# Performance work log

Measured on AMD Instinct MI355X. Metric: run time of the kernel, lower is better.

## Reference

```python
import jax, jax.numpy as jnp
import numpy as np

B, V, FIN, COUT, K = 16, 20000, 64, 64, 16


def setup_inputs() -> dict:
    key = jax.random.key(0)
    k1, k2, k3, k4 = jax.random.split(key, 4)
    x = jax.random.normal(k1, (B, V, FIN), dtype=jnp.float32)
    Wx = jax.random.normal(k2, (FIN, COUT), dtype=jnp.float32) * (1.0 / np.sqrt(FIN))
    Wn = jax.random.normal(k3, (FIN, COUT), dtype=jnp.float32) * (1.0 / np.sqrt(FIN))
    b = jnp.zeros((COUT,), dtype=jnp.float32)
    # neighbor indices into the padded input: 0 is the zero-padding row, 1..V are real vertices
    neighbor = jax.random.randint(k4, (V, K), 0, V + 1, dtype=jnp.int32)
    return {"x": x, "Wx": Wx, "Wn": Wn, "b": b, "neighbor": neighbor}


def reference(x, Wx, Wn, b, neighbor):
    # x: [B, V, Fin]; neighbor: [V, K] indices into padded (V+1) vertex axis
    Bsz, Vn, Fin = x.shape
    pad = jnp.zeros((Bsz, 1, Fin), dtype=x.dtype)
    padded = jnp.concatenate([pad, x], axis=1)            # [B, V+1, Fin]
    nb = padded[:, neighbor, :]                            # [B, V, K, Fin] (gather)
    nb_mean = jnp.mean(nb, axis=2)                         # sum/K == mean (zeros included)
    out = jnp.einsum('bvf,fc->bvc', x, Wx) \
        + jnp.einsum('bvf,fc->bvc', nb_mean, Wn) + b
    return out
```

## Files before the change

kernel.cpp:

```cpp
#include <hip/hip_runtime.h>
#include <hip/hip_bf16.h>

#define BATCH 16
#define NV    20000
#define FIN   64
#define NCOUT 64
#define NK    16
#define TOTROWS  (BATCH * NV)
#define NTILES   (TOTROWS / 16)
#define TPX      (NTILES / 8)

typedef __attribute__((ext_vector_type(8))) short bf16x8;
typedef __attribute__((ext_vector_type(4))) float f32x4;
typedef __attribute__((ext_vector_type(4))) unsigned short u16x4;

__device__ __forceinline__ short f2b(float f) {
    __hip_bfloat16 h = __float2bfloat16(f);
    return __builtin_bit_cast(short, h);
}

__global__ __launch_bounds__(256, 4) void convnet_gemm(
    const float* __restrict__ x,
    const float* __restrict__ Wx,
    const float* __restrict__ Wn,
    const float* __restrict__ bias,
    __hip_bfloat16* __restrict__ z,
    float* __restrict__ out)
{
    const int lane = threadIdx.x & 63;
    const int m    = lane & 15;
    const int quad = lane >> 4;

    bf16x8 bf[8][2];
#pragma unroll
    for (int t = 0; t < 8; ++t) {
        const float* W = (t < 4) ? Wx : Wn;
        const float scale = (t < 4) ? 1.0f : (1.0f / 16.0f);
        const int c = 4 * m + (t & 3);
#pragma unroll
        for (int h = 0; h < 2; ++h) {
            bf16x8 fr;
#pragma unroll
            for (int j = 0; j < 8; ++j) {
                const int f = 32 * h + quad * 8 + j;
                fr[j] = f2b(W[f * NCOUT + c] * scale);
            }
            bf[t][h] = fr;
        }
    }
    float bias_q[4];
#pragma unroll
    for (int t = 0; t < 4; ++t) bias_q[t] = bias[4 * m + t];

    const int xcd = blockIdx.x & 7;
    const int bi  = blockIdx.x >> 3;
    const int wl  = bi * 4 + ((int)threadIdx.x >> 6);
    const int WPX = (gridDim.x >> 3) * 4;

    for (int t0 = wl; t0 < TPX; t0 += WPX) {
        const int rt = __builtin_amdgcn_readfirstlane(xcd * TPX + t0);
        const float* xt =
            x + (size_t)rt * (16 * FIN) + (size_t)m * FIN + quad * 8;

        const float4 La0 = ((const float4*)xt)[0];
        const float4 La1 = ((const float4*)xt)[1];
        const float4 Lb0 = ((const float4*)(xt + 32))[0];
        const float4 Lb1 = ((const float4*)(xt + 32))[1];

        bf16x8 af0, af1;
        af0[0] = f2b(La0.x); af0[1] = f2b(La0.y); af0[2] = f2b(La0.z); af0[3] = f2b(La0.w);
        af0[4] = f2b(La1.x); af0[5] = f2b(La1.y); af0[6] = f2b(La1.z); af0[7] = f2b(La1.w);
        af1[0] = f2b(Lb0.x); af1[1] = f2b(Lb0.y); af1[2] = f2b(Lb0.z); af1[3] = f2b(Lb0.w);
        af1[4] = f2b(Lb1.x); af1[5] = f2b(Lb1.y); af1[6] = f2b(Lb1.z); af1[7] = f2b(Lb1.w);

        const size_t rbase = (size_t)rt * 16 + quad * 4;

        {
            f32x4 accP[4];
#pragma unroll
            for (int t = 0; t < 4; ++t) accP[t] = (f32x4){0.f, 0.f, 0.f, 0.f};
#pragma unroll
            for (int t = 0; t < 4; ++t)
                accP[t] = __builtin_amdgcn_mfma_f32_16x16x32_bf16(af0, bf[t][0], accP[t], 0, 0, 0);
#pragma unroll
            for (int t = 0; t < 4; ++t)
                accP[t] = __builtin_amdgcn_mfma_f32_16x16x32_bf16(af1, bf[t][1], accP[t], 0, 0, 0);
#pragma unroll
            for (int r = 0; r < 4; ++r) {
                const size_t orow = (rbase + r) * NCOUT + 4 * m;
                float4 o;
                o.x = accP[0][r] + bias_q[0];
                o.y = accP[1][r] + bias_q[1];
                o.z = accP[2][r] + bias_q[2];
                o.w = accP[3][r] + bias_q[3];
                *(float4*)(out + orow) = o;
            }
        }
        {
            f32x4 accZ[4];
#pragma unroll
            for (int t = 0; t < 4; ++t) accZ[t] = (f32x4){0.f, 0.f, 0.f, 0.f};
#pragma unroll
            for (int t = 0; t < 4; ++t)
                accZ[t] = __builtin_amdgcn_mfma_f32_16x16x32_bf16(af0, bf[t + 4][0], accZ[t], 0, 0, 0);
#pragma unroll
            for (int t = 0; t < 4; ++t)
                accZ[t] = __builtin_amdgcn_mfma_f32_16x16x32_bf16(af1, bf[t + 4][1], accZ[t], 0, 0, 0);
#pragma unroll
            for (int r = 0; r < 4; ++r) {
                const size_t orow = (rbase + r) * NCOUT + 4 * m;
                u16x4 zz;
                zz.x = (unsigned short)f2b(accZ[0][r]);
                zz.y = (unsigned short)f2b(accZ[1][r]);
                zz.z = (unsigned short)f2b(accZ[2][r]);
                zz.w = (unsigned short)f2b(accZ[3][r]);
                *(u16x4*)(z + orow) = zz;
            }
        }
    }
}

__global__ __launch_bounds__(256, 8) void convnet_gather(
    const int* __restrict__ nbr,
    const __hip_bfloat16* __restrict__ z,
    float* __restrict__ out)
{
    const int lane = threadIdx.x & 63;
    const int s    = lane >> 4;
    const int c    = lane & 15;
    const int xcd  = blockIdx.x & 7;
    const int bi   = blockIdx.x >> 3;
    const int wl   = bi * 4 + ((int)threadIdx.x >> 6);
    const int WPX  = (gridDim.x >> 3) * 4;

    const int zcol   = c * 8;
    const int GROUPS = (2 * NV) / 4;

    for (int g = wl; g < GROUPS; g += WPX) {
        const int gu = __builtin_amdgcn_readfirstlane(g);
        const int bl = (gu >= NV / 4) ? 1 : 0;
        const int b  = 2 * xcd + bl;
        const int v0 = gu * 4 - bl * NV;
        const int row0 = b * NV + v0;

        float4* o = (float4*)(out + (size_t)(row0 + s) * NCOUT + 4 * c);
        float4 ov = *o;

        const int4* nb4 =
            (const int4*)((const char*)nbr + (size_t)(v0 + s) * (NK * 4));
        const int4 i0 = nb4[0];
        const int4 i1 = nb4[1];
        const int4 i2 = nb4[2];
        const int4 i3 = nb4[3];
        int id[NK];
        id[0] = i0.x; id[1] = i0.y; id[2]  = i0.z; id[3]  = i0.w;
        id[4] = i1.x; id[5] = i1.y; id[6]  = i1.z; id[7]  = i1.w;
        id[8] = i2.x; id[9] = i2.y; id[10] = i2.z; id[11] = i2.w;
        id[12] = i3.x; id[13] = i3.y; id[14] = i3.z; id[15] = i3.w;

        const char* zb = (const char*)z + (size_t)b * NV * 128;
        float a0 = 0.f, a1 = 0.f, a2 = 0.f, a3 = 0.f;
#pragma unroll
        for (int k = 0; k < NK; ++k) {
            const int idx = id[k];
            int sel = idx - 1;
            sel = sel < 0 ? 0 : sel;
            const uint2 d = *(const uint2*)(zb + (size_t)(unsigned)(sel * 128 + zcol));
            const unsigned dx = idx ? d.x : 0u;
            const unsigned dy = idx ? d.y : 0u;
            a0 += __builtin_bit_cast(float, dx << 16);
            a1 += __builtin_bit_cast(float, dx & 0xFFFF0000u);
            a2 += __builtin_bit_cast(float, dy << 16);
            a3 += __builtin_bit_cast(float, dy & 0xFFFF0000u);
        }

        ov.x += a0; ov.y += a1; ov.z += a2; ov.w += a3;
        *o = ov;
    }
}

extern "C" void kernel_launch(void* const* d_in, const int* in_sizes, int n_in,
                              void* d_out, int out_size, void* d_ws, size_t ws_size,
                              hipStream_t stream) {
    const float* x    = (const float*)d_in[0];
    const float* Wx   = (const float*)d_in[1];
    const float* Wn   = (const float*)d_in[2];
    const float* bias = (const float*)d_in[3];
    const int*   nbr  = (const int*)d_in[4];
    float* out = (float*)d_out;

    __hip_bfloat16* z = (__hip_bfloat16*)d_ws;

    hipLaunchKernelGGL(convnet_gemm, dim3(1024), dim3(256), 0, stream,
                       x, Wx, Wn, bias, z, out);
    hipLaunchKernelGGL(convnet_gather, dim3(2048), dim3(256), 0, stream,
                       nbr, z, out);
}
```

Baseline: 232.1 us.

## Fuse gather into Wx GEMM pass, split z precompute into separate kernel

Splits work into a z-only pass (x·Wn/16 stored as bf16) and a fused kernel that recomputes x·Wx, gathers neighbor z rows, adds bias and writes out once. This removes the intermediate write and re-read of the fp32 output between kernels, at the cost of reading x twice. Loads and stores of streaming data use nontemporal hints, and the fused kernel walks tiles in reverse order, perhaps to hit cache on recently read x. Mixing the gather with MFMA work in one kernel may cut occupancy or latency hiding.

Result: slower. 269.9 us (+16.3%).

```diff
diff --git a/kernel.cpp b/kernel.cpp
--- a/kernel.cpp
+++ b/kernel.cpp
@@ -9,43 +9,113 @@
 #define TOTROWS  (BATCH * NV)
 #define NTILES   (TOTROWS / 16)
 #define TPX      (NTILES / 8)
+#define TPB      (NV / 16)
 
 typedef __attribute__((ext_vector_type(8))) short bf16x8;
 typedef __attribute__((ext_vector_type(4))) float f32x4;
 typedef __attribute__((ext_vector_type(4))) unsigned short u16x4;
+typedef __attribute__((ext_vector_type(2))) unsigned int u32x2;
 
 __device__ __forceinline__ short f2b(float f) {
     __hip_bfloat16 h = __float2bfloat16(f);
     return __builtin_bit_cast(short, h);
 }
 
-__global__ __launch_bounds__(256, 4) void convnet_gemm(
+__global__ __launch_bounds__(256, 4) void convnet_zpass(
+    const float* __restrict__ x,
+    const float* __restrict__ Wn,
+    __hip_bfloat16* __restrict__ z)
+{
+    const int lane = threadIdx.x & 63;
+    const int m    = lane & 15;
+    const int quad = lane >> 4;
+
+    bf16x8 bn[4][2];
+#pragma unroll
+    for (int t = 0; t < 4; ++t) {
+        const int c = 4 * m + t;
+#pragma unroll
+        for (int h = 0; h < 2; ++h) {
+            bf16x8 fr;
+#pragma unroll
+            for (int j = 0; j < 8; ++j) {
+                const int f = 32 * h + quad * 8 + j;
+                fr[j] = f2b(Wn[f * NCOUT + c] * (1.0f / 16.0f));
+            }
+            bn[t][h] = fr;
+        }
+    }
+
+    const int xcd = blockIdx.x & 7;
+    const int bi  = blockIdx.x >> 3;
+    const int wl  = bi * 4 + ((int)threadIdx.x >> 6);
+    const int WPX = (gridDim.x >> 3) * 4;
+
+    for (int t0 = wl; t0 < TPX; t0 += WPX) {
+        const int rt = __builtin_amdgcn_readfirstlane(xcd * TPX + t0);
+        const float* xt =
+            x + (size_t)rt * (16 * FIN) + (size_t)m * FIN + quad * 8;
+
+        const f32x4 La0 = __builtin_nontemporal_load((const f32x4*)xt);
+        const f32x4 La1 = __builtin_nontemporal_load((const f32x4*)xt + 1);
+        const f32x4 Lb0 = __builtin_nontemporal_load((const f32x4*)(xt + 32));
+        const f32x4 Lb1 = __builtin_nontemporal_load((const f32x4*)(xt + 32) + 1);
+
+        bf16x8 af0, af1;
+        af0[0] = f2b(La0.x); af0[1] = f2b(La0.y); af0[2] = f2b(La0.z); af0[3] = f2b(La0.w);
+        af0[4] = f2b(La1.x); af0[5] = f2b(La1.y); af0[6] = f2b(La1.z); af0[7] = f2b(La1.w);
+        af1[0] = f2b(Lb0.x); af1[1] = f2b(Lb0.y); af1[2] = f2b(Lb0.z); af1[3] = f2b(Lb0.w);
+        af1[4] = f2b(Lb1.x); af1[5] = f2b(Lb1.y); af1[6] = f2b(Lb1.z); af1[7] = f2b(Lb1.w);
+
+        f32x4 acc[4];
+#pragma unroll
+        for (int t = 0; t < 4; ++t) acc[t] = (f32x4){0.f, 0.f, 0.f, 0.f};
+#pragma unroll
+        for (int t = 0; t < 4; ++t)
+            acc[t] = __builtin_amdgcn_mfma_f32_16x16x32_bf16(af0, bn[t][0], acc[t], 0, 0, 0);
+#pragma unroll
+        for (int t = 0; t < 4; ++t)
+            acc[t] = __builtin_amdgcn_mfma_f32_16x16x32_bf16(af1, bn[t][1], acc[t], 0, 0, 0);
+
+        const size_t rbase = (size_t)rt * 16 + quad * 4;
+#pragma unroll
+        for (int r = 0; r < 4; ++r) {
+            const size_t orow = (rbase + r) * NCOUT + 4 * m;
+            u16x4 zz;
+            zz.x = (unsigned short)f2b(acc[0][r]);
+            zz.y = (unsigned short)f2b(acc[1][r]);
+            zz.z = (unsigned short)f2b(acc[2][r]);
+            zz.w = (unsigned short)f2b(acc[3][r]);
+            *(u16x4*)(z + orow) = zz;
+        }
+    }
+}
+
+__global__ __launch_bounds__(256, 4) void convnet_fused(
     const float* __restrict__ x,
     const float* __restrict__ Wx,
-    const float* __restrict__ Wn,
     const float* __restrict__ bias,
-    __hip_bfloat16* __restrict__ z,
+    const int* __restrict__ nbr,
+    const __hip_bfloat16* __restrict__ z,
     float* __restrict__ out)
 {
     const int lane = threadIdx.x & 63;
     const int m    = lane & 15;
     const int quad = lane >> 4;
 
-    bf16x8 bf[8][2];
-#pragma unroll
-    for (int t = 0; t < 8; ++t) {
-        const float* W = (t < 4) ? Wx : Wn;
-        const float scale = (t < 4) ? 1.0f : (1.0f / 16.0f);
-        const int c = 4 * m + (t & 3);
+    bf16x8 bx[4][2];
+#pragma unroll
+    for (int t = 0; t < 4; ++t) {
+        const int c = 4 * m + t;
 #pragma unroll
         for (int h = 0; h < 2; ++h) {
             bf16x8 fr;
 #pragma unroll
             for (int j = 0; j < 8; ++j) {
                 const int f = 32 * h + quad * 8 + j;
-                fr[j] = f2b(W[f * NCOUT + c] * scale);
+                fr[j] = f2b(Wx[f * NCOUT + c]);
             }
-            bf[t][h] = fr;
+            bx[t][h] = fr;
         }
     }
     float bias_q[4];
@@ -57,15 +127,19 @@
     const int wl  = bi * 4 + ((int)threadIdx.x >> 6);
     const int WPX = (gridDim.x >> 3) * 4;
 
-    for (int t0 = wl; t0 < TPX; t0 += WPX) {
-        const int rt = __builtin_amdgcn_readfirstlane(xcd * TPX + t0);
+    for (int t0 = TPX - 1 - wl; t0 >= 0; t0 -= WPX) {
+        const int t0u = __builtin_amdgcn_readfirstlane(t0);
+        const int rt  = xcd * TPX + t0u;
+        const int blh = (t0u >= TPB) ? 1 : 0;
+        const int b   = 2 * xcd + blh;
+        const int v0  = (t0u - blh * TPB) * 16;
+
         const float* xt =
             x + (size_t)rt * (16 * FIN) + (size_t)m * FIN + quad * 8;
-
-        const float4 La0 = ((const float4*)xt)[0];
-        const float4 La1 = ((const float4*)xt)[1];
-        const float4 Lb0 = ((const float4*)(xt + 32))[0];
-        const float4 Lb1 = ((const float4*)(xt + 32))[1];
+        const f32x4 La0 = __builtin_nontemporal_load((const f32x4*)xt);
+        const f32x4 La1 = __builtin_nontemporal_load((const f32x4*)xt + 1);
+        const f32x4 Lb0 = __builtin_nontemporal_load((const f32x4*)(xt + 32));
+        const f32x4 Lb1 = __builtin_nontemporal_load((const f32x4*)(xt + 32) + 1);
 
         bf16x8 af0, af1;
         af0[0] = f2b(La0.x); af0[1] = f2b(La0.y); af0[2] = f2b(La0.z); af0[3] = f2b(La0.w);
@@ -73,109 +147,64 @@
         af1[0] = f2b(Lb0.x); af1[1] = f2b(Lb0.y); af1[2] = f2b(Lb0.z); af1[3] = f2b(Lb0.w);
         af1[4] = f2b(Lb1.x); af1[5] = f2b(Lb1.y); af1[6] = f2b(Lb1.z); af1[7] = f2b(Lb1.w);
 
+        f32x4 acc[4];
+#pragma unroll
+        for (int t = 0; t < 4; ++t) acc[t] = (f32x4){0.f, 0.f, 0.f, 0.f};
+#pragma unroll
+        for (int t = 0; t < 4; ++t)
+            acc[t] = __builtin_amdgcn_mfma_f32_16x16x32_bf16(af0, bx[t][0], acc[t], 0, 0, 0);
+#pragma unroll
+        for (int t = 0; t < 4; ++t)
+            acc[t] = __builtin_amdgcn_mfma_f32_16x16x32_bf16(af1, bx[t][1], acc[t], 0, 0, 0);
+
+        const char* zb = (const char*)z + (size_t)b * (NV * 128);
+        const int zcol = m * 8;
+#pragma unroll
+        for (int r = 0; r < 4; ++r) {
+            const int v = v0 + quad * 4 + r;
+            const int4* nb4 = (const int4*)nbr + (size_t)v * 4;
+            const int4 i0 = nb4[0];
+            const int4 i1 = nb4[1];
+            const int4 i2 = nb4[2];
+            const int4 i3 = nb4[3];
+            int id[NK];
+            id[0]  = i0.x; id[1]  = i0.y; id[2]  = i0.z; id[3]  = i0.w;
+            id[4]  = i1.x; id[5]  = i1.y; id[6]  = i1.z; id[7]  = i1.w;
+            id[8]  = i2.x; id[9]  = i2.y; id[10] = i2.z; id[11] = i2.w;
+            id[12] = i3.x; id[13] = i3.y; id[14] = i3.z; id[15] = i3.w;
+
+            float a0 = 0.f, a1 = 0.f, a2 = 0.f, a3 = 0.f;
+#pragma unroll
+            for (int k = 0; k < NK; ++k) {
+                const int idx = id[k];
+                int sel = idx - 1;
+                sel = sel < 0 ? 0 : sel;
+                const u32x2 d =
+                    *(const u32x2*)(zb + (size_t)(unsigned)(sel * 128 + zcol));
+                const unsigned dx = idx ? d.x : 0u;
+                const unsigned dy = idx ? d.y : 0u;
+                a0 += __builtin_bit_cast(float, dx << 16);
+                a1 += __builtin_bit_cast(float, dx & 0xFFFF0000u);
+                a2 += __builtin_bit_cast(float, dy << 16);
+                a3 += __builtin_bit_cast(float, dy & 0xFFFF0000u);
+            }
+            acc[0][r] += a0;
+            acc[1][r] += a1;
+            acc[2][r] += a2;
+            acc[3][r] += a3;
+        }
+
         const size_t rbase = (size_t)rt * 16 + quad * 4;
-
-        {
-            f32x4 accP[4];
-#pragma unroll
-            for (int t = 0; t < 4; ++t) accP[t] = (f32x4){0.f, 0.f, 0.f, 0.f};
-#pragma unroll
-            for (int t = 0; t < 4; ++t)
-                accP[t] = __builtin_amdgcn_mfma_f32_16x16x32_bf16(af0, bf[t][0], accP[t], 0, 0, 0);
-#pragma unroll
-            for (int t = 0; t < 4; ++t)
-                accP[t] = __builtin_amdgcn_mfma_f32_16x16x32_bf16(af1, bf[t][1], accP[t], 0, 0, 0);
-#pragma unroll
-            for (int r = 0; r < 4; ++r) {
-                const size_t orow = (rbase + r) * NCOUT + 4 * m;
-                float4 o;
-                o.x = accP[0][r] + bias_q[0];
-                o.y = accP[1][r] + bias_q[1];
-                o.z = accP[2][r] + bias_q[2];
-                o.w = accP[3][r] + bias_q[3];
-                *(float4*)(out + orow) = o;
-            }
-        }
-        {
-            f32x4 accZ[4];
-#pragma unroll
-            for (int t = 0; t < 4; ++t) accZ[t] = (f32x4){0.f, 0.f, 0.f, 0.f};
-#pragma unroll
-            for (int t = 0; t < 4; ++t)
-                accZ[t] = __builtin_amdgcn_mfma_f32_16x16x32_bf16(af0, bf[t + 4][0], accZ[t], 0, 0, 0);
-#pragma unroll
-            for (int t = 0; t < 4; ++t)
-                accZ[t] = __builtin_amdgcn_mfma_f32_16x16x32_bf16(af1, bf[t + 4][1], accZ[t], 0, 0, 0);
-#pragma unroll
-            for (int r = 0; r < 4; ++r) {
-                const size_t orow = (rbase + r) * NCOUT + 4 * m;
-                u16x4 zz;
-                zz.x = (unsigned short)f2b(accZ[0][r]);
-                zz.y = (unsigned short)f2b(accZ[1][r]);
-                zz.z = (unsigned short)f2b(accZ[2][r]);
-                zz.w = (unsigned short)f2b(accZ[3][r]);
-                *(u16x4*)(z + orow) = zz;
-            }
-        }
-    }
-}
-
-__global__ __launch_bounds__(256, 8) void convnet_gather(
-    const int* __restrict__ nbr,
-    const __hip_bfloat16* __restrict__ z,
-    float* __restrict__ out)
-{
-    const int lane = threadIdx.x & 63;
-    const int s    = lane >> 4;
-    const int c    = lane & 15;
-    const int xcd  = blockIdx.x & 7;
-    const int bi   = blockIdx.x >> 3;
-    const int wl   = bi * 4 + ((int)threadIdx.x >> 6);
-    const int WPX  = (gridDim.x >> 3) * 4;
-
-    const int zcol   = c * 8;
-    const int GROUPS = (2 * NV) / 4;
-
-    for (int g = wl; g < GROUPS; g += WPX) {
-        const int gu = __builtin_amdgcn_readfirstlane(g);
-        const int bl = (gu >= NV / 4) ? 1 : 0;
-        const int b  = 2 * xcd + bl;
-        const int v0 = gu * 4 - bl * NV;
-        const int row0 = b * NV + v0;
-
-        float4* o = (float4*)(out + (size_t)(row0 + s) * NCOUT + 4 * c);
-        float4 ov = *o;
-
-        const int4* nb4 =
-            (const int4*)((const char*)nbr + (size_t)(v0 + s) * (NK * 4));
-        const int4 i0 = nb4[0];
-        const int4 i1 = nb4[1];
-        const int4 i2 = nb4[2];
-        const int4 i3 = nb4[3];
-        int id[NK];
-        id[0] = i0.x; id[1] = i0.y; id[2]  = i0.z; id[3]  = i0.w;
-        id[4] = i1.x; id[5] = i1.y; id[6]  = i1.z; id[7]  = i1.w;
-        id[8] = i2.x; id[9] = i2.y; id[10] = i2.z; id[11] = i2.w;
-        id[12] = i3.x; id[13] = i3.y; id[14] = i3.z; id[15] = i3.w;
-
-        const char* zb = (const char*)z + (size_t)b * NV * 128;
-        float a0 = 0.f, a1 = 0.f, a2 = 0.f, a3 = 0.f;
-#pragma unroll
-        for (int k = 0; k < NK; ++k) {
-            const int idx = id[k];
-            int sel = idx - 1;
-            sel = sel < 0 ? 0 : sel;
-            const uint2 d = *(const uint2*)(zb + (size_t)(unsigned)(sel * 128 + zcol));
-            const unsigned dx = idx ? d.x : 0u;
-            const unsigned dy = idx ? d.y : 0u;
-            a0 += __builtin_bit_cast(float, dx << 16);
-            a1 += __builtin_bit_cast(float, dx & 0xFFFF0000u);
-            a2 += __builtin_bit_cast(float, dy << 16);
-            a3 += __builtin_bit_cast(float, dy & 0xFFFF0000u);
-        }
-
-        ov.x += a0; ov.y += a1; ov.z += a2; ov.w += a3;
-        *o = ov;
+#pragma unroll
+        for (int r = 0; r < 4; ++r) {
+            const size_t orow = (rbase + r) * NCOUT + 4 * m;
+            f32x4 o;
+            o.x = acc[0][r] + bias_q[0];
+            o.y = acc[1][r] + bias_q[1];
+            o.z = acc[2][r] + bias_q[2];
+            o.w = acc[3][r] + bias_q[3];
+            __builtin_nontemporal_store(o, (f32x4*)(out + orow));
+        }
     }
 }
 
@@ -191,8 +220,8 @@
 
     __hip_bfloat16* z = (__hip_bfloat16*)d_ws;
 
-    hipLaunchKernelGGL(convnet_gemm, dim3(1024), dim3(256), 0, stream,
-                       x, Wx, Wn, bias, z, out);
-    hipLaunchKernelGGL(convnet_gather, dim3(2048), dim3(256), 0, stream,
-                       nbr, z, out);
-}
+    hipLaunchKernelGGL(convnet_zpass, dim3(1024), dim3(256), 0, stream,
+                       x, Wn, z);
+    hipLaunchKernelGGL(convnet_fused, dim3(1024), dim3(256), 0, stream,
+                       x, Wx, bias, nbr, z, out);
+}
```
